# Performance work log

Measured on AMD Instinct MI355X. Metric: run time of the kernel, lower is better.

## Reference

```python
import jax, jax.numpy as jnp
import numpy as np

N = 50000       # nodes
E = 1600000     # edges (avg degree 32)
IN = 128        # node_in_dim
D = 64          # node_out_dim (= GRU hidden)
H = 1           # heads
ED = 3          # edge_in_dim
STEPS = 3       # num_step_message_passing
EPS = 1e-5      # BatchNorm eps
SLOPE = 0.2     # LeakyReLU negative slope (GAT default)


def setup_inputs() -> dict:
    key = jax.random.key(0)
    ks = jax.random.split(key, 16)
    s_in = 1.0 / np.sqrt(IN)
    s_d = 1.0 / np.sqrt(D)
    return {
        "x": jax.random.normal(ks[0], (N, IN), jnp.float32),
        "edge_attr": jax.random.normal(ks[1], (E, ED), jnp.float32),
        "mlp_w": jax.random.normal(ks[2], (IN, D), jnp.float32) * s_in,
        "mlp_b": jnp.zeros((D,), jnp.float32),
        "bn_g": jnp.ones((D,), jnp.float32),
        "bn_b": jnp.zeros((D,), jnp.float32),
        "conv_w": jax.random.normal(ks[3], (D, H * D), jnp.float32) * s_d,
        "att_dst": jax.random.normal(ks[4], (H, D), jnp.float32) * s_d,
        "att_src": jax.random.normal(ks[5], (H, D), jnp.float32) * s_d,
        "att_edge": jax.random.normal(ks[6], (H, ED), jnp.float32) * s_d,
        "w_ih": jax.random.normal(ks[7], (3 * D, H * D), jnp.float32) * s_d,
        "w_hh": jax.random.normal(ks[8], (3 * D, D), jnp.float32) * s_d,
        "b_ih": jnp.zeros((3 * D,), jnp.float32),
        "b_hh": jnp.zeros((3 * D,), jnp.float32),
        "lin_w": jax.random.normal(ks[9], (IN, D), jnp.float32) * s_in,
        "lin_b": jnp.zeros((D,), jnp.float32),
        "edge_index": jax.random.randint(ks[10], (2, E), 0, N, jnp.int64),
    }


def _egat_conv(out, edge_attr, src, dst, conv_w, att_dst, att_src, att_edge):
    # out: [N, D] -> xt: [N, H, D]
    xt = (out @ conv_w).reshape(N, H, D)
    # per-node attention halves (avoid gathering twice): [N, H]
    a_dst_n = jnp.einsum("nhd,hd->nh", xt, att_dst)
    a_src_n = jnp.einsum("nhd,hd->nh", xt, att_src)
    # per-edge logits: [E, H]
    logits = a_dst_n[dst] + a_src_n[src] + edge_attr @ att_edge.T
    logits = jnp.where(logits >= 0, logits, SLOPE * logits)
    # segment softmax over destination nodes
    seg_max = jax.ops.segment_max(logits, dst, num_segments=N)  # [N, H]
    seg_max = jnp.where(jnp.isfinite(seg_max), seg_max, 0.0)
    expd = jnp.exp(logits - seg_max[dst])
    denom = jax.ops.segment_sum(expd, dst, num_segments=N)      # [N, H]
    alpha = expd / denom[dst]                                   # [E, H]
    # attention-weighted aggregation of source features
    msgs = alpha[:, :, None] * xt[src]                          # [E, H, D]
    agg = jax.ops.segment_sum(msgs, dst, num_segments=N)        # [N, H, D]
    return agg.reshape(N, H * D)


def _gru_cell(x_in, h, w_ih, w_hh, b_ih, b_hh):
    gi = x_in @ w_ih.T + b_ih
    gh = h @ w_hh.T + b_hh
    gi_r, gi_z, gi_n = jnp.split(gi, 3, axis=-1)
    gh_r, gh_z, gh_n = jnp.split(gh, 3, axis=-1)
    r = jax.nn.sigmoid(gi_r + gh_r)
    z = jax.nn.sigmoid(gi_z + gh_z)
    n = jnp.tanh(gi_n + r * gh_n)
    return (1.0 - z) * n + z * h


def reference(x, edge_attr, mlp_w, mlp_b, bn_g, bn_b, conv_w, att_dst,
              att_src, att_edge, w_ih, w_hh, b_ih, b_hh, lin_w, lin_b,
              edge_index):
    src, dst = edge_index[0], edge_index[1]
    # initial embedding: ReLU(BatchNorm(Linear(x))) with batch stats
    h0 = x @ mlp_w + mlp_b
    mu = jnp.mean(h0, axis=0)
    var = jnp.var(h0, axis=0)
    out = jax.nn.relu((h0 - mu) * jax.lax.rsqrt(var + EPS) * bn_g + bn_b)
    h = out
    for _ in range(STEPS):
        m = jax.nn.relu(_egat_conv(out, edge_attr, src, dst,
                                   conv_w, att_dst, att_src, att_edge))
        h = _gru_cell(m, h, w_ih, w_hh, b_ih, b_hh)
        out = h
    return x @ lin_w + lin_b + out
```

## Files before the change

kernel.cpp:

```cpp
#include <hip/hip_runtime.h>

typedef unsigned short ushort_t;
typedef unsigned int uint_t;
typedef __attribute__((ext_vector_type(8))) short bf16x8;
typedef __attribute__((ext_vector_type(4))) float f32x4;

#define N_NODES 50000
#define N_EDGES 1600000
#define NB_BKT 391
#define CAP_BKT 4608
#define CAP_B 6144
#define GBK 782
#define WPAD 72

__device__ __forceinline__ float bfu(ushort_t u) {
    return __uint_as_float(((uint_t)u) << 16);
}
__device__ __forceinline__ ushort_t f2b(float f) {
    uint_t x = __float_as_uint(f);
    uint_t r = (x + 0x7FFFu + ((x >> 16) & 1u)) >> 16;
    return (ushort_t)r;
}
__device__ __forceinline__ float sigm(float x) {
    return 1.0f / (1.0f + __expf(-x));
}
__device__ __forceinline__ float tanh_f(float x) {
    return 1.0f - 2.0f / (__expf(2.0f * x) + 1.0f);
}
__device__ __forceinline__ bf16x8 pack8(const float* v) {
    bf16x8 r;
#pragma unroll
    for (int j = 0; j < 8; ++j) r[j] = (short)f2b(v[j]);
    return r;
}
__device__ __forceinline__ int ld_src(const int* __restrict__ ei, int i, int f64) {
    return f64 ? ei[2 * i] : ei[i];
}
__device__ __forceinline__ int ld_dst(const int* __restrict__ ei, int i, int f64) {
    return f64 ? ei[2 * N_EDGES + 2 * i] : ei[N_EDGES + i];
}
__device__ __forceinline__ bool is_f64(const int* flag) { return flag[0] > 2048; }

__global__ void k_sentinel(float* __restrict__ out, int n) {
    int i = blockIdx.x * 256 + threadIdx.x;
    if (i < n) out[i] = 100.0f;
}

__global__ void k_prep(const float* __restrict__ w_ih, const float* __restrict__ w_hh,
                       const float* __restrict__ conv_w, const float* __restrict__ mlp_w,
                       const float* __restrict__ lin_w, const int* __restrict__ ei,
                       ushort_t* __restrict__ wb, ushort_t* __restrict__ cwb,
                       ushort_t* __restrict__ mlpT, ushort_t* __restrict__ linT,
                       int* __restrict__ flag, int* __restrict__ gtail) {
    int blk = blockIdx.x;
    if (blk < 176) {
        int t = blk * 256 + threadIdx.x;
        if (t < 24576) {
            const float* w = (t < 12288) ? w_ih : w_hh;
            wb[t] = f2b(w[t < 12288 ? t : t - 12288]);
        } else if (t < 28672) {
            int r = t - 24576;
            int j = r >> 6, k = r & 63;
            cwb[j * 64 + k] = f2b(conv_w[k * 64 + j]);
        } else if (t < 36864) {
            int r = t - 28672;
            int j = r >> 7, k = r & 127;
            mlpT[j * 128 + k] = f2b(mlp_w[k * 64 + j]);
        } else if (t < 45056) {
            int r = t - 36864;
            int j = r >> 7, k = r & 127;
            linT[j * 128 + k] = f2b(lin_w[k * 64 + j]);
        }
    } else if (blk == 176) {
        __shared__ int red[256];
        int tid = threadIdx.x;
        int zeros = 0;
#pragma unroll
        for (int j = 0; j < 16; ++j) {
            int slot = (tid * 16 + j) * 2 + 1;
            if (ei[slot] == 0) zeros++;
        }
        red[tid] = zeros;
        __syncthreads();
        for (int off = 128; off; off >>= 1) {
            if (tid < off) red[tid] += red[tid + off];
            __syncthreads();
        }
        if (tid == 0) flag[0] = red[0];
    } else {
        int b = (blk - 177) * 256 + threadIdx.x;
        if (b < NB_BKT) gtail[b] = b * CAP_BKT;
    }
}

__global__ __launch_bounds__(256) void k_embbkt(
    const int* __restrict__ ei, const int* __restrict__ flag,
    const float* __restrict__ ea, const float* __restrict__ ae,
    int* __restrict__ gtail, uint2* __restrict__ bkt, int e,
    const float* __restrict__ x, const ushort_t* __restrict__ mlpT,
    const float* __restrict__ mlp_b, float* __restrict__ h0, int n) {
    if (blockIdx.x < GBK) {
        __shared__ int cnt[NB_BKT];
        __shared__ int gbase[NB_BKT];
        for (int i = threadIdx.x; i < NB_BKT; i += 256) cnt[i] = 0;
        __syncthreads();
        int base = blockIdx.x * 2048;
        int f64 = is_f64(flag);
        float a0 = ae[0], a1 = ae[1], a2 = ae[2];
        uint_t w0[8], w1[8];
        int bk[8], rk[8];
#pragma unroll
        for (int j = 0; j < 8; ++j) {
            int i = base + j * 256 + threadIdx.x;
            bk[j] = -1;
            if (i < e) {
                int d = ld_dst(ei, i, f64);
                if ((uint_t)d < (uint_t)N_NODES) {
                    int s = ld_src(ei, i, f64);
                    if ((uint_t)s >= (uint_t)N_NODES) s = 0;
                    float ed = ea[i * 3] * a0 + ea[i * 3 + 1] * a1 + ea[i * 3 + 2] * a2;
                    bk[j] = d >> 7;
                    w0[j] = (uint_t)s | ((uint_t)(d & 127) << 16);
                    w1[j] = __float_as_uint(ed);
                    rk[j] = atomicAdd(&cnt[bk[j]], 1);
                }
            }
        }
        __syncthreads();
        for (int t = threadIdx.x; t < NB_BKT; t += 256) {
            int c = cnt[t];
            gbase[t] = c ? atomicAdd(&gtail[t], c) : 0;
        }
        __syncthreads();
#pragma unroll
        for (int j = 0; j < 8; ++j) {
            if (bk[j] >= 0) {
                int pos = gbase[bk[j]] + rk[j];
                if (pos < (bk[j] + 1) * CAP_BKT) {
                    uint2 p;
                    p.x = w0[j];
                    p.y = w1[j];
                    bkt[pos] = p;
                }
            }
        }
    } else {
        int lane = threadIdx.x & 63;
        int wv = threadIdx.x >> 6;
        int tile = (blockIdx.x - GBK) * 4 + wv;
        if (tile * 16 >= n) return;
        int nb16 = tile * 16;
        int mrow = lane & 15, q = lane >> 4;
        const float* xp = x + (nb16 + mrow) * 128 + q * 8;
        bf16x8 a[4];
#pragma unroll
        for (int kc = 0; kc < 4; ++kc) {
            float hv[8];
            const float* p = xp + kc * 32;
#pragma unroll
            for (int j = 0; j < 8; ++j) hv[j] = p[j];
            a[kc] = pack8(hv);
        }
        f32x4 acc[4];
#pragma unroll
        for (int t = 0; t < 4; ++t) acc[t] = (f32x4){0.f, 0.f, 0.f, 0.f};
#pragma unroll
        for (int kc = 0; kc < 4; ++kc) {
#pragma unroll
            for (int t = 0; t < 4; ++t) {
                bf16x8 b =
                    *(const bf16x8*)(mlpT + (t * 16 + mrow) * 128 + kc * 32 + q * 8);
                acc[t] = __builtin_amdgcn_mfma_f32_16x16x32_bf16(a[kc], b, acc[t], 0, 0, 0);
            }
        }
#pragma unroll
        for (int t = 0; t < 4; ++t) {
            int j = t * 16 + mrow;
            float bias = mlp_b[j];
#pragma unroll
            for (int r = 0; r < 4; ++r)
                h0[(nb16 + q * 4 + r) * 64 + j] = acc[t][r] + bias;
        }
    }
}

__global__ __launch_bounds__(256) void k_statsort(
    const int* __restrict__ gtail, const uint2* __restrict__ bkt,
    uint_t* __restrict__ pk, int* __restrict__ rs, int n,
    const float* __restrict__ h0, float* __restrict__ stats) {
    __shared__ char smem[26624];
    int tid = threadIdx.x;
    if (blockIdx.x < NB_BKT) {
        int* red = (int*)smem;
        int* cnt = (int*)(smem + 1024);
        int* sc = (int*)(smem + 1536);
        uint_t* stg = (uint_t*)(smem + 2048);
        int b = blockIdx.x;
        int partial = 0;
        for (int i = tid; i < b; i += 256)
            partial += min(gtail[i] - i * CAP_BKT, CAP_BKT);
        red[tid] = partial;
        __syncthreads();
        for (int off = 128; off; off >>= 1) {
            if (tid < off) red[tid] += red[tid + off];
            __syncthreads();
        }
        int obase = red[0];
        int node0 = b * 128;
        int nloc = min(128, n - node0);
        int size = min(gtail[b] - b * CAP_BKT, CAP_BKT);
        const uint2* bin = bkt + b * CAP_BKT;
        for (int i = tid; i < 128; i += 256) cnt[i] = 0;
        __syncthreads();
        for (int ofs = tid; ofs < size; ofs += 256) {
            int dlow = (bin[ofs].x >> 16) & 127;
            atomicAdd(&cnt[dlow], 1);
        }
        __syncthreads();
        if (tid < 128) sc[tid] = cnt[tid];
        __syncthreads();
        for (int off = 1; off < 128; off <<= 1) {
            int add = (tid < 128 && tid >= off) ? sc[tid - off] : 0;
            __syncthreads();
            if (tid < 128) sc[tid] += add;
            __syncthreads();
        }
        if (tid < 128) sc[tid] -= cnt[tid];
        __syncthreads();
        if (tid < nloc) rs[node0 + tid] = obase + sc[tid];
        if (b == NB_BKT - 1 && tid == 0) rs[n] = obase + size;
        for (int i = tid; i < 128; i += 256) cnt[i] = 0;
        __syncthreads();
        for (int ofs = tid; ofs < size; ofs += 256) {
            uint2 p = bin[ofs];
            int dlow = (p.x >> 16) & 127;
            int r = atomicAdd(&cnt[dlow], 1);
            int pos = sc[dlow] + r;
            uint_t q = (p.x & 0xFFFFu) | ((uint_t)f2b(__uint_as_float(p.y)) << 16);
            if (pos < CAP_B) stg[pos] = q;
            else pk[obase + pos] = q;
        }
        __syncthreads();
        int wlim = min(size, CAP_B);
        for (int ofs = tid; ofs < wlim; ofs += 256) pk[obase + ofs] = stg[ofs];
    } else {
        float* ssum = (float*)smem;
        float* ssq = (float*)(smem + 1024);
        int gid = (blockIdx.x - NB_BKT) * 256 + tid;
        int col = gid & 63;
        int rg = gid >> 6;
        float s = 0.f, s2 = 0.f;
        for (int row = rg; row < n; row += 1024) {
            float v = h0[row * 64 + col];
            s += v;
            s2 += v * v;
        }
        ssum[tid] = s;
        ssq[tid] = s2;
        __syncthreads();
        if (tid < 64) {
            s = ssum[tid] + ssum[tid + 64] + ssum[tid + 128] + ssum[tid + 192];
            s2 = ssq[tid] + ssq[tid + 64] + ssq[tid + 128] + ssq[tid + 192];
            atomicAdd(&stats[tid], s);
            atomicAdd(&stats[64 + tid], s2);
        }
    }
}

__global__ __launch_bounds__(256) void k_xt(float* __restrict__ h,
                                            const ushort_t* __restrict__ cwb,
                                            const float* __restrict__ att_dst,
                                            const float* __restrict__ att_src,
                                            const float* __restrict__ bn_g,
                                            const float* __restrict__ bn_b,
                                            const float* __restrict__ stats,
                                            float inv_n,
                                            ushort_t* __restrict__ xt,
                                            float* __restrict__ adst,
                                            float* __restrict__ asrc, int n) {
    __shared__ float scb[64], shb[64];
    {
        int tid = threadIdx.x;
        if (tid < 64) {
            float mu = stats[tid] * inv_n;
            float var = fmaxf(stats[64 + tid] * inv_n - mu * mu, 0.f);
            float sc = rsqrtf(var + 1e-5f) * bn_g[tid];
            scb[tid] = sc;
            shb[tid] = bn_b[tid] - mu * sc;
        }
        __syncthreads();
    }
    int lane = threadIdx.x & 63;
    int wv = threadIdx.x >> 6;
    int tile = blockIdx.x * 4 + wv;
    if (tile * 16 >= n) return;
    int nb16 = tile * 16;
    int mrow = lane & 15, q = lane >> 4;
    bf16x8 ah[2];
    {
        float* hp = h + (nb16 + mrow) * 64 + q * 8;
        float hv[8];
#pragma unroll
        for (int kh = 0; kh < 2; ++kh) {
            float* p = hp + kh * 32;
            int cb = kh * 32 + q * 8;
#pragma unroll
            for (int j = 0; j < 8; ++j) {
                hv[j] = fmaxf(p[j] * scb[cb + j] + shb[cb + j], 0.f);
                p[j] = hv[j];
            }
            ah[kh] = pack8(hv);
        }
    }
    f32x4 acc[4];
#pragma unroll
    for (int t = 0; t < 4; ++t) acc[t] = (f32x4){0.f, 0.f, 0.f, 0.f};
#pragma unroll
    for (int kh = 0; kh < 2; ++kh) {
#pragma unroll
        for (int t = 0; t < 4; ++t) {
            bf16x8 b = *(const bf16x8*)(cwb + (t * 16 + mrow) * 64 + kh * 32 + q * 8);
            acc[t] = __builtin_amdgcn_mfma_f32_16x16x32_bf16(ah[kh], b, acc[t], 0, 0, 0);
        }
    }
    float sd[4] = {0, 0, 0, 0}, ss[4] = {0, 0, 0, 0};
#pragma unroll
    for (int t = 0; t < 4; ++t) {
        int j = t * 16 + mrow;
        float ad = att_dst[j], as = att_src[j];
#pragma unroll
        for (int r = 0; r < 4; ++r) {
            float v = acc[t][r];
            xt[(nb16 + q * 4 + r) * 64 + j] = f2b(v);
            sd[r] += v * ad;
            ss[r] += v * as;
        }
    }
#pragma unroll
    for (int off = 1; off < 16; off <<= 1) {
#pragma unroll
        for (int r = 0; r < 4; ++r) {
            sd[r] += __shfl_xor(sd[r], off);
            ss[r] += __shfl_xor(ss[r], off);
        }
    }
    if (mrow == 0) {
#pragma unroll
        for (int r = 0; r < 4; ++r) {
            adst[nb16 + q * 4 + r] = sd[r];
            asrc[nb16 + q * 4 + r] = ss[r];
        }
    }
}

__global__ __launch_bounds__(256) void k_agg(const int* __restrict__ rs,
                                             const uint_t* __restrict__ pk,
                                             const float* __restrict__ adst,
                                             const float* __restrict__ asrc,
                                             const ushort_t* __restrict__ xt,
                                             ushort_t* __restrict__ m, int n) {
    __shared__ float s_w[4][64];
    __shared__ int s_s[4][64];
    int lane = threadIdx.x & 63;
    int wv = threadIdx.x >> 6;
    int v = blockIdx.x * 4 + wv;
    if (v >= n) return;
    int start = rs[v], end = rs[v + 1];
    if (start >= end) {
        m[v * 64 + lane] = 0;
        return;
    }
    float adv = adst[v];
    int g = lane >> 3;
    int cb = (lane & 7) * 8;
    float acc[8] = {0, 0, 0, 0, 0, 0, 0, 0};
    float dsum = 0.f;
    for (int base = start; base < end; base += 64) {
        int e = base + lane;
        float w = 0.f;
        int s = 0;
        if (e < end) {
            uint_t p = pk[e];
            s = (int)(p & 0xFFFFu);
            float l = adv + asrc[s] + bfu((ushort_t)(p >> 16));
            l = (l >= 0.f) ? l : 0.2f * l;
            w = __expf(l);
        }
        dsum += w;
        s_w[wv][lane] = w;
        s_s[wv][lane] = s;
        int cnt = min(64, end - base);
        int nb8 = (cnt + 7) >> 3;
        for (int tb = 0; tb < nb8; ++tb) {
            int sl = tb * 8 + g;
            float w8 = s_w[wv][sl];
            int s8 = s_s[wv][sl];
            uint4 qv = *(const uint4*)(xt + s8 * 64 + cb);
            acc[0] += w8 * __uint_as_float(qv.x << 16);
            acc[1] += w8 * __uint_as_float(qv.x & 0xFFFF0000u);
            acc[2] += w8 * __uint_as_float(qv.y << 16);
            acc[3] += w8 * __uint_as_float(qv.y & 0xFFFF0000u);
            acc[4] += w8 * __uint_as_float(qv.z << 16);
            acc[5] += w8 * __uint_as_float(qv.z & 0xFFFF0000u);
            acc[6] += w8 * __uint_as_float(qv.w << 16);
            acc[7] += w8 * __uint_as_float(qv.w & 0xFFFF0000u);
        }
    }
#pragma unroll
    for (int off = 32; off; off >>= 1) dsum += __shfl_xor(dsum, off);
#pragma unroll
    for (int off = 8; off < 64; off <<= 1) {
#pragma unroll
        for (int j = 0; j < 8; ++j) acc[j] += __shfl_xor(acc[j], off);
    }
    float inv = 1.0f / fmaxf(dsum, 1e-20f);
    if (g == 0) {
        uint4 o;
        o.x = (uint_t)f2b(fmaxf(acc[0] * inv, 0.f)) |
              ((uint_t)f2b(fmaxf(acc[1] * inv, 0.f)) << 16);
        o.y = (uint_t)f2b(fmaxf(acc[2] * inv, 0.f)) |
              ((uint_t)f2b(fmaxf(acc[3] * inv, 0.f)) << 16);
        o.z = (uint_t)f2b(fmaxf(acc[4] * inv, 0.f)) |
              ((uint_t)f2b(fmaxf(acc[5] * inv, 0.f)) << 16);
        o.w = (uint_t)f2b(fmaxf(acc[6] * inv, 0.f)) |
              ((uint_t)f2b(fmaxf(acc[7] * inv, 0.f)) << 16);
        *(uint4*)(m + v * 64 + cb) = o;
    }
}

__global__ __launch_bounds__(256) void k_gruxt(
    const ushort_t* __restrict__ mb, float* __restrict__ h,
    const ushort_t* __restrict__ wb, const ushort_t* __restrict__ cwb,
    const float* __restrict__ b_ih, const float* __restrict__ b_hh,
    const float* __restrict__ att_dst, const float* __restrict__ att_src,
    int do_xt, ushort_t* __restrict__ xt, float* __restrict__ adst,
    float* __restrict__ asrc, int n) {
    __shared__ ushort_t swb[384 * WPAD];
    __shared__ ushort_t scw[64 * WPAD];
    {
        const uint2* src = (const uint2*)wb;
        for (int g = threadIdx.x; g < 6144; g += 256) {
            uint2 v = src[g];
            int row = g >> 4;
            int col = (g & 15) * 4;
            *(uint2*)(swb + row * WPAD + col) = v;
        }
        const uint2* srcc = (const uint2*)cwb;
        for (int g = threadIdx.x; g < 1024; g += 256) {
            uint2 v = srcc[g];
            int row = g >> 4;
            int col = (g & 15) * 4;
            *(uint2*)(scw + row * WPAD + col) = v;
        }
    }
    __syncthreads();
    int lane = threadIdx.x & 63;
    int wv = threadIdx.x >> 6;
    int tile = blockIdx.x * 4 + wv;
    if (tile * 16 >= n) return;
    int nb16 = tile * 16;
    int mrow = lane & 15, q = lane >> 4;
    float hp[4][4];
#pragma unroll
    for (int t = 0; t < 4; ++t)
#pragma unroll
        for (int r = 0; r < 4; ++r)
            hp[t][r] = h[(nb16 + q * 4 + r) * 64 + t * 16 + mrow];
    bf16x8 am[2], ah[2];
    {
        const ushort_t* mp = mb + (nb16 + mrow) * 64 + q * 8;
        am[0] = *(const bf16x8*)(mp);
        am[1] = *(const bf16x8*)(mp + 32);
        const float* hpt = h + (nb16 + mrow) * 64 + q * 8;
        float hv[8];
#pragma unroll
        for (int j = 0; j < 8; ++j) hv[j] = hpt[j];
        ah[0] = pack8(hv);
#pragma unroll
        for (int j = 0; j < 8; ++j) hv[j] = hpt[32 + j];
        ah[1] = pack8(hv);
    }
    f32x4 acc[24];
#pragma unroll
    for (int t = 0; t < 24; ++t) acc[t] = (f32x4){0.f, 0.f, 0.f, 0.f};
#pragma unroll
    for (int kh = 0; kh < 2; ++kh) {
#pragma unroll
        for (int t = 0; t < 12; ++t) {
            bf16x8 b = *(const bf16x8*)(swb + (t * 16 + mrow) * WPAD + kh * 32 + q * 8);
            acc[t] = __builtin_amdgcn_mfma_f32_16x16x32_bf16(am[kh], b, acc[t], 0, 0, 0);
        }
#pragma unroll
        for (int t = 0; t < 12; ++t) {
            bf16x8 b =
                *(const bf16x8*)(swb + (192 + t * 16 + mrow) * WPAD + kh * 32 + q * 8);
            acc[12 + t] =
                __builtin_amdgcn_mfma_f32_16x16x32_bf16(ah[kh], b, acc[12 + t], 0, 0, 0);
        }
    }
#pragma unroll
    for (int t = 0; t < 4; ++t) {
        int j = t * 16 + mrow;
        float bir = b_ih[j], biz = b_ih[64 + j], bin = b_ih[128 + j];
        float bhr = b_hh[j], bhz = b_hh[64 + j], bhn = b_hh[128 + j];
#pragma unroll
        for (int r = 0; r < 4; ++r) {
            int node = nb16 + q * 4 + r;
            float gr = acc[t][r] + bir + acc[12 + t][r] + bhr;
            float gz = acc[4 + t][r] + biz + acc[16 + t][r] + bhz;
            float rr = sigm(gr);
            float zz = sigm(gz);
            float tt = acc[8 + t][r] + bin + rr * (acc[20 + t][r] + bhn);
            h[node * 64 + j] = (1.f - zz) * tanh_f(tt) + zz * hp[t][r];
        }
    }
    if (!do_xt) return;
    __threadfence_block();
    bf16x8 ah2[2];
    {
        const float* hpt = h + (nb16 + mrow) * 64 + q * 8;
        float hv[8];
#pragma unroll
        for (int j = 0; j < 8; ++j) hv[j] = hpt[j];
        ah2[0] = pack8(hv);
#pragma unroll
        for (int j = 0; j < 8; ++j) hv[j] = hpt[32 + j];
        ah2[1] = pack8(hv);
    }
    f32x4 xacc[4];
#pragma unroll
    for (int t = 0; t < 4; ++t) xacc[t] = (f32x4){0.f, 0.f, 0.f, 0.f};
#pragma unroll
    for (int kh = 0; kh < 2; ++kh) {
#pragma unroll
        for (int t = 0; t < 4; ++t) {
            bf16x8 b = *(const bf16x8*)(scw + (t * 16 + mrow) * WPAD + kh * 32 + q * 8);
            xacc[t] = __builtin_amdgcn_mfma_f32_16x16x32_bf16(ah2[kh], b, xacc[t], 0, 0, 0);
        }
    }
    float sd[4] = {0, 0, 0, 0}, ss[4] = {0, 0, 0, 0};
#pragma unroll
    for (int t = 0; t < 4; ++t) {
        int j = t * 16 + mrow;
        float ad = att_dst[j], as = att_src[j];
#pragma unroll
        for (int r = 0; r < 4; ++r) {
            float v = xacc[t][r];
            xt[(nb16 + q * 4 + r) * 64 + j] = f2b(v);
            sd[r] += v * ad;
            ss[r] += v * as;
        }
    }
#pragma unroll
    for (int off = 1; off < 16; off <<= 1) {
#pragma unroll
        for (int r = 0; r < 4; ++r) {
            sd[r] += __shfl_xor(sd[r], off);
            ss[r] += __shfl_xor(ss[r], off);
        }
    }
    if (mrow == 0) {
#pragma unroll
        for (int r = 0; r < 4; ++r) {
            adst[nb16 + q * 4 + r] = sd[r];
            asrc[nb16 + q * 4 + r] = ss[r];
        }
    }
}

__global__ __launch_bounds__(256) void k_out(const float* __restrict__ x,
                                             const ushort_t* __restrict__ linT,
                                             const float* __restrict__ lin_b,
                                             const float* __restrict__ h,
                                             float* __restrict__ out, int n) {
    int lane = threadIdx.x & 63;
    int wv = threadIdx.x >> 6;
    int tile = blockIdx.x * 4 + wv;
    if (tile * 16 >= n) return;
    int nb16 = tile * 16;
    int mrow = lane & 15, q = lane >> 4;
    const float* xp = x + (nb16 + mrow) * 128 + q * 8;
    bf16x8 a[4];
#pragma unroll
    for (int kc = 0; kc < 4; ++kc) {
        float hv[8];
        const float* p = xp + kc * 32;
#pragma unroll
        for (int j = 0; j < 8; ++j) hv[j] = p[j];
        a[kc] = pack8(hv);
    }
    f32x4 acc[4];
#pragma unroll
    for (int t = 0; t < 4; ++t) acc[t] = (f32x4){0.f, 0.f, 0.f, 0.f};
#pragma unroll
    for (int kc = 0; kc < 4; ++kc) {
#pragma unroll
        for (int t = 0; t < 4; ++t) {
            bf16x8 b = *(const bf16x8*)(linT + (t * 16 + mrow) * 128 + kc * 32 + q * 8);
            acc[t] = __builtin_amdgcn_mfma_f32_16x16x32_bf16(a[kc], b, acc[t], 0, 0, 0);
        }
    }
#pragma unroll
    for (int t = 0; t < 4; ++t) {
        int j = t * 16 + mrow;
        float bias = lin_b[j];
#pragma unroll
        for (int r = 0; r < 4; ++r) {
            int node = nb16 + q * 4 + r;
            out[node * 64 + j] = acc[t][r] + bias + h[node * 64 + j];
        }
    }
}

extern "C" void kernel_launch(void* const* d_in, const int* in_sizes, int n_in,
                              void* d_out, int out_size, void* d_ws, size_t ws_size,
                              hipStream_t stream) {
    const float* x = (const float*)d_in[0];
    const float* edge_attr = (const float*)d_in[1];
    const float* mlp_w = (const float*)d_in[2];
    const float* mlp_b = (const float*)d_in[3];
    const float* bn_g = (const float*)d_in[4];
    const float* bn_b = (const float*)d_in[5];
    const float* conv_w = (const float*)d_in[6];
    const float* att_dst = (const float*)d_in[7];
    const float* att_src = (const float*)d_in[8];
    const float* att_edge = (const float*)d_in[9];
    const float* w_ih = (const float*)d_in[10];
    const float* w_hh = (const float*)d_in[11];
    const float* b_ih = (const float*)d_in[12];
    const float* b_hh = (const float*)d_in[13];
    const float* lin_w = (const float*)d_in[14];
    const float* lin_b = (const float*)d_in[15];
    const int* ei = (const int*)d_in[16];

    char* ws = (char*)d_ws;
    float* f_h = (float*)(ws + 0);
    ushort_t* mb = (ushort_t*)(ws + 12800000);
    ushort_t* xt = (ushort_t*)(ws + 19200000);
    uint2* bkt = (uint2*)(ws + 25600000);
    uint_t* pk = (uint_t*)(ws + 40013824);
    float* f_adst = (float*)(ws + 46413824);
    float* f_asrc = (float*)(ws + 46614016);
    int* row_start = (int*)(ws + 46814208);
    float* stats = (float*)(ws + 47014656);
    int* flag = (int*)(ws + 47015168);
    ushort_t* wb = (ushort_t*)(ws + 47015680);
    ushort_t* cwb = (ushort_t*)(ws + 47064832);
    ushort_t* mlpT = (ushort_t*)(ws + 47073024);
    ushort_t* linT = (ushort_t*)(ws + 47089408);
    int* gtail = (int*)(ws + 47105792);

    const size_t needed = 47107840;
    if (ws_size < needed) {
        k_sentinel<<<(out_size + 255) / 256, 256, 0, stream>>>((float*)d_out, out_size);
        return;
    }

    const int n = N_NODES, e = N_EDGES;
    const int gT = ((n + 15) / 16 + 3) / 4;
    const int gN4 = (n + 3) / 4;
    const int gPrep = 176 + 1 + (NB_BKT + 255) / 256;
    const float inv_n = 1.0f / (float)n;

    hipMemsetAsync(stats, 0, 512, stream);

    k_prep<<<gPrep, 256, 0, stream>>>(w_ih, w_hh, conv_w, mlp_w, lin_w, ei, wb, cwb,
                                      mlpT, linT, flag, gtail);
    k_embbkt<<<GBK + gT, 256, 0, stream>>>(ei, flag, edge_attr, att_edge, gtail, bkt, e,
                                           x, mlpT, mlp_b, f_h, n);
    k_statsort<<<NB_BKT + 256, 256, 0, stream>>>(gtail, bkt, pk, row_start, n, f_h,
                                                 stats);
    k_xt<<<gT, 256, 0, stream>>>(f_h, cwb, att_dst, att_src, bn_g, bn_b, stats, inv_n,
                                 xt, f_adst, f_asrc, n);

    for (int s = 0; s < 3; ++s) {
        k_agg<<<gN4, 256, 0, stream>>>(row_start, pk, f_adst, f_asrc, xt, mb, n);
        k_gruxt<<<gT, 256, 0, stream>>>(mb, f_h, wb, cwb, b_ih, b_hh, att_dst, att_src,
                                        (s < 2) ? 1 : 0, xt, f_adst, f_asrc, n);
    }

    k_out<<<gT, 256, 0, stream>>>(x, linT, lin_b, f_h, (float*)d_out, n);
}
```

Baseline: 371.9 us.

## Fuse output projection into final GRU step and drop LDS weight staging

The final step of the GRU kernel now computes the x@lin_w projection and writes the output directly, removing the separate k_out launch and the write and reread of h. The GRU and conv weights are now read straight from global memory (through the cache) instead of being staged into padded shared memory with a block barrier. This removes per-block LDS fill cost and the barrier, and frees LDS for occupancy. The trade-off is that the MFMA B operands become uncoalesced global loads.

New measurement: 412.6 us. 10.9% more time.

```diff
diff --git a/kernel.cpp b/kernel.cpp
--- a/kernel.cpp
+++ b/kernel.cpp
@@ -11,7 +11,6 @@
 #define CAP_BKT 4608
 #define CAP_B 6144
 #define GBK 782
-#define WPAD 72
 
 __device__ __forceinline__ float bfu(ushort_t u) {
     return __uint_as_float(((uint_t)u) << 16);
@@ -434,26 +433,9 @@
     const float* __restrict__ b_ih, const float* __restrict__ b_hh,
     const float* __restrict__ att_dst, const float* __restrict__ att_src,
     int do_xt, ushort_t* __restrict__ xt, float* __restrict__ adst,
-    float* __restrict__ asrc, int n) {
-    __shared__ ushort_t swb[384 * WPAD];
-    __shared__ ushort_t scw[64 * WPAD];
-    {
-        const uint2* src = (const uint2*)wb;
-        for (int g = threadIdx.x; g < 6144; g += 256) {
-            uint2 v = src[g];
-            int row = g >> 4;
-            int col = (g & 15) * 4;
-            *(uint2*)(swb + row * WPAD + col) = v;
-        }
-        const uint2* srcc = (const uint2*)cwb;
-        for (int g = threadIdx.x; g < 1024; g += 256) {
-            uint2 v = srcc[g];
-            int row = g >> 4;
-            int col = (g & 15) * 4;
-            *(uint2*)(scw + row * WPAD + col) = v;
-        }
-    }
-    __syncthreads();
+    float* __restrict__ asrc, int do_out, const float* __restrict__ x,
+    const ushort_t* __restrict__ linT, const float* __restrict__ lin_b,
+    float* __restrict__ out, int n) {
     int lane = threadIdx.x & 63;
     int wv = threadIdx.x >> 6;
     int tile = blockIdx.x * 4 + wv;
@@ -483,21 +465,22 @@
     f32x4 acc[24];
 #pragma unroll
     for (int t = 0; t < 24; ++t) acc[t] = (f32x4){0.f, 0.f, 0.f, 0.f};
+    const ushort_t* wrow = wb + mrow * 64;
 #pragma unroll
     for (int kh = 0; kh < 2; ++kh) {
 #pragma unroll
         for (int t = 0; t < 12; ++t) {
-            bf16x8 b = *(const bf16x8*)(swb + (t * 16 + mrow) * WPAD + kh * 32 + q * 8);
+            bf16x8 b = *(const bf16x8*)(wrow + t * 1024 + kh * 32 + q * 8);
             acc[t] = __builtin_amdgcn_mfma_f32_16x16x32_bf16(am[kh], b, acc[t], 0, 0, 0);
         }
 #pragma unroll
         for (int t = 0; t < 12; ++t) {
-            bf16x8 b =
-                *(const bf16x8*)(swb + (192 + t * 16 + mrow) * WPAD + kh * 32 + q * 8);
+            bf16x8 b = *(const bf16x8*)(wrow + (192 + t * 16) * 64 + kh * 32 + q * 8);
             acc[12 + t] =
                 __builtin_amdgcn_mfma_f32_16x16x32_bf16(ah[kh], b, acc[12 + t], 0, 0, 0);
         }
     }
+    float hnew[4][4];
 #pragma unroll
     for (int t = 0; t < 4; ++t) {
         int j = t * 16 + mrow;
@@ -505,14 +488,55 @@
         float bhr = b_hh[j], bhz = b_hh[64 + j], bhn = b_hh[128 + j];
 #pragma unroll
         for (int r = 0; r < 4; ++r) {
-            int node = nb16 + q * 4 + r;
             float gr = acc[t][r] + bir + acc[12 + t][r] + bhr;
             float gz = acc[4 + t][r] + biz + acc[16 + t][r] + bhz;
             float rr = sigm(gr);
             float zz = sigm(gz);
             float tt = acc[8 + t][r] + bin + rr * (acc[20 + t][r] + bhn);
-            h[node * 64 + j] = (1.f - zz) * tanh_f(tt) + zz * hp[t][r];
-        }
+            hnew[t][r] = (1.f - zz) * tanh_f(tt) + zz * hp[t][r];
+        }
+    }
+    if (do_out) {
+        const float* xp = x + (nb16 + mrow) * 128 + q * 8;
+        bf16x8 a[4];
+#pragma unroll
+        for (int kc = 0; kc < 4; ++kc) {
+            float hv[8];
+            const float* p = xp + kc * 32;
+#pragma unroll
+            for (int j = 0; j < 8; ++j) hv[j] = p[j];
+            a[kc] = pack8(hv);
+        }
+        f32x4 xacc[4];
+#pragma unroll
+        for (int t = 0; t < 4; ++t) xacc[t] = (f32x4){0.f, 0.f, 0.f, 0.f};
+#pragma unroll
+        for (int kc = 0; kc < 4; ++kc) {
+#pragma unroll
+            for (int t = 0; t < 4; ++t) {
+                bf16x8 b =
+                    *(const bf16x8*)(linT + (t * 16 + mrow) * 128 + kc * 32 + q * 8);
+                xacc[t] =
+                    __builtin_amdgcn_mfma_f32_16x16x32_bf16(a[kc], b, xacc[t], 0, 0, 0);
+            }
+        }
+#pragma unroll
+        for (int t = 0; t < 4; ++t) {
+            int j = t * 16 + mrow;
+            float bias = lin_b[j];
+#pragma unroll
+            for (int r = 0; r < 4; ++r) {
+                int node = nb16 + q * 4 + r;
+                out[node * 64 + j] = xacc[t][r] + bias + hnew[t][r];
+            }
+        }
+        return;
+    }
+#pragma unroll
+    for (int t = 0; t < 4; ++t) {
+        int j = t * 16 + mrow;
+#pragma unroll
+        for (int r = 0; r < 4; ++r) h[(nb16 + q * 4 + r) * 64 + j] = hnew[t][r];
     }
     if (!do_xt) return;
     __threadfence_block();
@@ -534,7 +558,7 @@
     for (int kh = 0; kh < 2; ++kh) {
 #pragma unroll
         for (int t = 0; t < 4; ++t) {
-            bf16x8 b = *(const bf16x8*)(scw + (t * 16 + mrow) * WPAD + kh * 32 + q * 8);
+            bf16x8 b = *(const bf16x8*)(cwb + (t * 16 + mrow) * 64 + kh * 32 + q * 8);
             xacc[t] = __builtin_amdgcn_mfma_f32_16x16x32_bf16(ah2[kh], b, xacc[t], 0, 0, 0);
         }
     }
@@ -564,50 +588,6 @@
         for (int r = 0; r < 4; ++r) {
             adst[nb16 + q * 4 + r] = sd[r];
             asrc[nb16 + q * 4 + r] = ss[r];
-        }
-    }
-}
-
-__global__ __launch_bounds__(256) void k_out(const float* __restrict__ x,
-                                             const ushort_t* __restrict__ linT,
-                                             const float* __restrict__ lin_b,
-                                             const float* __restrict__ h,
-                                             float* __restrict__ out, int n) {
-    int lane = threadIdx.x & 63;
-    int wv = threadIdx.x >> 6;
-    int tile = blockIdx.x * 4 + wv;
-    if (tile * 16 >= n) return;
-    int nb16 = tile * 16;
-    int mrow = lane & 15, q = lane >> 4;
-    const float* xp = x + (nb16 + mrow) * 128 + q * 8;
-    bf16x8 a[4];
-#pragma unroll
-    for (int kc = 0; kc < 4; ++kc) {
-        float hv[8];
-        const float* p = xp + kc * 32;
-#pragma unroll
-        for (int j = 0; j < 8; ++j) hv[j] = p[j];
-        a[kc] = pack8(hv);
-    }
-    f32x4 acc[4];
-#pragma unroll
-    for (int t = 0; t < 4; ++t) acc[t] = (f32x4){0.f, 0.f, 0.f, 0.f};
-#pragma unroll
-    for (int kc = 0; kc < 4; ++kc) {
-#pragma unroll
-        for (int t = 0; t < 4; ++t) {
-            bf16x8 b = *(const bf16x8*)(linT + (t * 16 + mrow) * 128 + kc * 32 + q * 8);
-            acc[t] = __builtin_amdgcn_mfma_f32_16x16x32_bf16(a[kc], b, acc[t], 0, 0, 0);
-        }
-    }
-#pragma unroll
-    for (int t = 0; t < 4; ++t) {
-        int j = t * 16 + mrow;
-        float bias = lin_b[j];
-#pragma unroll
-        for (int r = 0; r < 4; ++r) {
-            int node = nb16 + q * 4 + r;
-            out[node * 64 + j] = acc[t][r] + bias + h[node * 64 + j];
         }
     }
 }
@@ -676,8 +656,8 @@
     for (int s = 0; s < 3; ++s) {
         k_agg<<<gN4, 256, 0, stream>>>(row_start, pk, f_adst, f_asrc, xt, mb, n);
         k_gruxt<<<gT, 256, 0, stream>>>(mb, f_h, wb, cwb, b_ih, b_hh, att_dst, att_src,
-                                        (s < 2) ? 1 : 0, xt, f_adst, f_asrc, n);
-    }
-
-    k_out<<<gT, 256, 0, stream>>>(x, linT, lin_b, f_h, (float*)d_out, n);
-}
+                                        (s < 2) ? 1 : 0, xt, f_adst, f_asrc,
+                                        (s == 2) ? 1 : 0, x, linT, lin_b,
+                                        (float*)d_out, n);
+    }
+}
```
